# Kernel tuning notes

Measured on AMD Instinct MI355X. Metric: run time of the kernel, lower is better.

Reference implementation:

```python
import jax, jax.numpy as jnp
import numpy as np


def setup_inputs() -> dict:
    key = jax.random.key(0)
    k1, k2 = jax.random.split(key)
    N, C, H, W = 8, 512, 64, 64
    K = 64
    x = jax.random.normal(k1, (N, C, H, W), dtype=jnp.float32)
    y = jax.random.normal(k2, (N, K, H, W), dtype=jnp.float32)
    scale = jnp.zeros((1,), dtype=jnp.float32)
    return {"x": x, "y": y, "scale": scale}


def reference(x, y, scale):
    N, C, H, W = x.shape
    K = y.shape[1]
    HW = H * W
    xq = x.reshape(N, C, HW)            # (N, C, HW) queries (channel-wise)
    yk = y.reshape(N, K, HW)            # (N, K, HW) keys/values
    # energy: (N, C, K)
    energy = jnp.einsum('ncs,nks->nck', xq, yk)
    # inverted max-subtraction: softmax(max_k(E) - E) over last dim
    energy_new = jnp.max(energy, axis=-1, keepdims=True) - energy
    attention = jax.nn.softmax(energy_new, axis=-1)  # (N, C, K)
    out = jnp.einsum('nck,nks->ncs', attention, yk)   # (N, C, HW)
    out = out.reshape(N, C, H, W)
    return x + scale * out
```

## Files before the change

kernel.cpp:

```cpp
#include <hip/hip_runtime.h>

#define N_ 8
#define C_ 512
#define K_ 64
#define HW_ 4096
#define SCHUNK 128
#define NCH 32

typedef __attribute__((ext_vector_type(8))) short short8;
typedef __attribute__((ext_vector_type(4))) float floatx4;

__device__ __forceinline__ short8 cvt8(const float* __restrict__ p){
  float4 u = *(const float4*)p;
  float4 w = *(const float4*)(p + 4);
  union { unsigned u32[4]; short8 s; } r;
  asm("v_cvt_pk_bf16_f32 %0, %1, %2" : "=v"(r.u32[0]) : "v"(u.x), "v"(u.y));
  asm("v_cvt_pk_bf16_f32 %0, %1, %2" : "=v"(r.u32[1]) : "v"(u.z), "v"(u.w));
  asm("v_cvt_pk_bf16_f32 %0, %1, %2" : "=v"(r.u32[2]) : "v"(w.x), "v"(w.y));
  asm("v_cvt_pk_bf16_f32 %0, %1, %2" : "=v"(r.u32[3]) : "v"(w.z), "v"(w.w));
  return r.s;
}

__device__ __forceinline__ void gload16(const void* g, void* l){
  __builtin_amdgcn_global_load_lds(
      (const __attribute__((address_space(1))) void*)g,
      (__attribute__((address_space(3))) void*)l, 16, 0, 0);
}

__global__ __launch_bounds__(256) void k_prep(const float* __restrict__ y,
                                              unsigned short* __restrict__ ybf,
                                              unsigned short* __restrict__ ytr){
  __shared__ unsigned short tile[64][72];
  int n  = blockIdx.x >> 6;
  int s0 = (blockIdx.x & 63) << 6;
  int tid = threadIdx.x;
  int k  = tid >> 2;
  int sc = (tid & 3) << 4;
  const float* yp = y + ((size_t)n * K_ + k) * HW_ + s0 + sc;
  union { unsigned short u16[16]; short8 s8[2]; uint4 q[2]; } u;
  u.s8[0] = cvt8(yp);
  u.s8[1] = cvt8(yp + 8);
  unsigned short* rp = ybf + ((size_t)n * K_ + k) * HW_ + s0 + sc;
  *(uint4*)rp       = u.q[0];
  *(uint4*)(rp + 8) = u.q[1];
#pragma unroll
  for (int j = 0; j < 16; ++j) tile[sc + j][k] = u.u16[j];
  __syncthreads();
  int s  = tid >> 2;
  int kc = (tid & 3) << 4;
  unsigned short* tp = ytr + ((size_t)n * HW_ + s0 + s) * K_ + kc;
  *(uint4*)tp       = *(const uint4*)&tile[s][kc];
  *(uint4*)(tp + 8) = *(const uint4*)&tile[s][kc + 8];
}

__global__ __launch_bounds__(1024) void k_fused(const float* __restrict__ x,
                                                const unsigned short* __restrict__ ybf,
                                                const unsigned short* __restrict__ ytr,
                                                const float* __restrict__ scale,
                                                float* __restrict__ out){
  __shared__ char smem[116736];

  const int bid = ((blockIdx.x & 7) << 5) | (blockIdx.x >> 3);
  const int ct = bid & 31, n = bid >> 5;
  const int tid = threadIdx.x;
  const int w = tid >> 6, l = tid & 63;
  const int lo = l & 15, hi = l >> 4;
  const int h = w >> 2, q = w & 3;
  const int c0 = ct << 4;

  float sc = scale[0];
  asm volatile("" :: "v"(sc));

  const int ar = l >> 3;
  const int ag = (l & 7) ^ ar;
  const char* asrc0 = (const char*)(x + ((size_t)n * C_ + c0 + 0 + ar) * HW_
                                    + h * 32 + ag * 4);
  const char* asrc1 = (const char*)(x + ((size_t)n * C_ + c0 + 8 + ar) * HW_
                                    + h * 32 + ag * 4);
  const int br = l >> 2;
  const int bg = (l & 3) ^ (br & 3);
  const char* bsrc = (const char*)(ybf + ((size_t)n * K_ + (q << 4) + br) * HW_
                                   + h * 32 + bg * 8);

  char* wbase = smem + w * 6144;
  floatx4 acc = {0.f, 0.f, 0.f, 0.f};

#define ESTG(BUF, CH)                                                          \
  {                                                                            \
    gload16(asrc0 + (size_t)(CH) * (SCHUNK * 4), wbase + (BUF) * 3072);        \
    gload16(asrc1 + (size_t)(CH) * (SCHUNK * 4), wbase + (BUF) * 3072 + 1024); \
    gload16(bsrc  + (size_t)(CH) * (SCHUNK * 2), wbase + (BUF) * 3072 + 2048); \
  }

#define ECMP(BUF)                                                              \
  {                                                                            \
    const char* Ab = wbase + (BUF) * 3072;                                     \
    float4 f0 = *(const float4*)(Ab + lo * 128 + (((hi << 1)       ^ (lo & 7)) << 4)); \
    float4 f1 = *(const float4*)(Ab + lo * 128 + ((((hi << 1) | 1) ^ (lo & 7)) << 4)); \
    union { unsigned u32[4]; short8 s; } xf;                                   \
    asm("v_cvt_pk_bf16_f32 %0, %1, %2" : "=v"(xf.u32[0]) : "v"(f0.x), "v"(f0.y)); \
    asm("v_cvt_pk_bf16_f32 %0, %1, %2" : "=v"(xf.u32[1]) : "v"(f0.z), "v"(f0.w)); \
    asm("v_cvt_pk_bf16_f32 %0, %1, %2" : "=v"(xf.u32[2]) : "v"(f1.x), "v"(f1.y)); \
    asm("v_cvt_pk_bf16_f32 %0, %1, %2" : "=v"(xf.u32[3]) : "v"(f1.z), "v"(f1.w)); \
    short8 yf = *(const short8*)(Ab + 2048 + lo * 64 + ((hi ^ (lo & 3)) << 4)); \
       \
    acc = __builtin_amdgcn_mfma_f32_16x16x32_bf16(yf, xf.s, acc, 0, 0, 0);     \
  }

  ESTG(0, 0) ESTG(1, 1)

  for (int cp = 0; cp < 15; ++cp){
    int ch = cp << 1;
    asm volatile("s_waitcnt vmcnt(3)" ::: "memory");
    ECMP(0)
    ESTG(0, ch + 2)
    asm volatile("s_waitcnt vmcnt(3)" ::: "memory");
    ECMP(1)
    ESTG(1, ch + 3)
  }
  asm volatile("s_waitcnt vmcnt(3)" ::: "memory");
  ECMP(0)
  asm volatile("s_waitcnt vmcnt(0)" ::: "memory");
  ECMP(1)
#undef ESTG
#undef ECMP

  float (*Els)[16][64] = (float (*)[16][64])(smem + 98304);
  *(floatx4*)&Els[h][lo][(q << 4) + (hi << 2)] = acc;
  __syncthreads();

  char* attl = smem + 114688;
  if (tid < 256){
    int c = tid >> 4, j = tid & 15;
    float4 t0 = *(const float4*)&Els[0][c][4 * j];
    float4 t1 = *(const float4*)&Els[1][c][4 * j];
    float4 t2 = *(const float4*)&Els[2][c][4 * j];
    float4 t3 = *(const float4*)&Els[3][c][4 * j];
    float e0 = t0.x + t1.x + t2.x + t3.x;
    float e1 = t0.y + t1.y + t2.y + t3.y;
    float e2 = t0.z + t1.z + t2.z + t3.z;
    float e3 = t0.w + t1.w + t2.w + t3.w;
    float m = fminf(fminf(e0, e1), fminf(e2, e3));
#pragma unroll
    for (int off = 8; off; off >>= 1) m = fminf(m, __shfl_xor(m, off, 16));
    float p0 = __expf(m - e0), p1 = __expf(m - e1);
    float p2 = __expf(m - e2), p3 = __expf(m - e3);
    float s = p0 + p1 + p2 + p3;
#pragma unroll
    for (int off = 8; off; off >>= 1) s += __shfl_xor(s, off, 16);
    float inv = 1.f / s;
    unsigned d0, d1;
    asm("v_cvt_pk_bf16_f32 %0, %1, %2" : "=v"(d0) : "v"(p0 * inv), "v"(p1 * inv));
    asm("v_cvt_pk_bf16_f32 %0, %1, %2" : "=v"(d1) : "v"(p2 * inv), "v"(p3 * inv));
    uint2 dd; dd.x = d0; dd.y = d1;
    *(uint2*)(attl + c * 128 + ((8 * j) ^ ((c & 7) << 4))) = dd;
  }
  __syncthreads();

  short8 batt0 = *(const short8*)(attl + lo * 128 + ((     hi * 16) ^ ((lo & 7) << 4)));
  short8 batt1 = *(const short8*)(attl + lo * 128 + ((64 + hi * 16) ^ ((lo & 7) << 4)));
  const unsigned short* ybn = ytr + (size_t)n * HW_ * K_;
  const int sP = w << 8;
  float (*Tw)[68] = (float (*)[68])(smem + w * 4352);
  size_t xb[4];
#pragma unroll
  for (int rg = 0; rg < 4; ++rg)
    xb[rg] = ((size_t)n * C_ + c0 + (rg << 2) + hi) * HW_ + sP + (lo << 2);

  short8 aA[8]; float4 xA[4];
  short8 aB[8]; float4 xB[4];

#define PVLOAD(G, AV, XV)                                                      \
  {                                                                            \
    int sg = sP + (G) * 64;                                                    \
    _Pragma("unroll")                                                          \
    for (int t = 0; t < 4; ++t){                                               \
      const unsigned short* ap = ybn + (size_t)(sg + t * 16 + lo) * K_ + (hi << 3); \
      AV[2 * t]     = *(const short8*)(ap);                                    \
      AV[2 * t + 1] = *(const short8*)(ap + 32);                               \
    }                                                                          \
    _Pragma("unroll")                                                          \
    for (int rg = 0; rg < 4; ++rg)                                             \
      XV[rg] = *(const float4*)(x + xb[rg] + (G) * 64);                        \
  }

#define PVCOMP(G, AV, XV)                                                      \
  {                                                                            \
    _Pragma("unroll")                                                          \
    for (int t = 0; t < 4; ++t){                                               \
      floatx4 a2 = {0.f, 0.f, 0.f, 0.f};                                       \
      a2 = __builtin_amdgcn_mfma_f32_16x16x32_bf16(AV[2 * t],     batt0, a2, 0, 0, 0); \
      a2 = __builtin_amdgcn_mfma_f32_16x16x32_bf16(AV[2 * t + 1], batt1, a2, 0, 0, 0); \
      *(floatx4*)&Tw[lo][t * 16 + (hi << 2)] = a2;    \
    }                                                                          \
    _Pragma("unroll")                                                          \
    for (int rg = 0; rg < 4; ++rg){                                            \
      float4 v  = *(const float4*)&Tw[(rg << 2) + hi][lo << 2];                \
      float4 xv = XV[rg];                                                      \
      float4 o;                                                                \
      o.x = xv.x + sc * v.x; o.y = xv.y + sc * v.y;                            \
      o.z = xv.z + sc * v.z; o.w = xv.w + sc * v.w;                            \
      *(float4*)(out + xb[rg] + (G) * 64) = o;                                 \
    }                                                                          \
  }

  PVLOAD(0, aA, xA)
  PVLOAD(1, aB, xB)
  PVCOMP(0, aA, xA)
  PVLOAD(2, aA, xA)
  PVCOMP(1, aB, xB)
  PVLOAD(3, aB, xB)
  PVCOMP(2, aA, xA)
  PVCOMP(3, aB, xB)
#undef PVLOAD
#undef PVCOMP
}

extern "C" void kernel_launch(void* const* d_in, const int* in_sizes, int n_in,
                              void* d_out, int out_size, void* d_ws, size_t ws_size,
                              hipStream_t stream){
  const float* x     = (const float*)d_in[0];
  const float* y     = (const float*)d_in[1];
  const float* scale = (const float*)d_in[2];
  float* out = (float*)d_out;

  char* ws = (char*)d_ws;
  unsigned short* ybf = (unsigned short*)(ws);
  unsigned short* ytr = (unsigned short*)(ws + (4u<<20));

  k_prep  <<<N_ * (HW_/64), 256,  0, stream>>>(y, ybf, ytr);
  k_fused <<<N_ * 32,       1024, 0, stream>>>(x, ybf, ytr, scale, out);
}
```

Measured before the change: 49.00 us.

## Split fused kernel into split-HW energy and parallel PV kernels

Replaces the single fused kernel (256 blocks of 1024 threads) with two kernels. The energy kernel splits the HW reduction into two halves and writes partial energies to workspace. A separate PV kernel with 2048 blocks of 256 threads sums the partials, computes the softmax, and applies the attention over eight HW slices. This aims to raise occupancy and parallelism across CUs, at the cost of an extra launch, a workspace round-trip, and softmax being recomputed by every slice block.

After: 49.92 us. About the same (+1.9%).

```diff
diff --git a/kernel.cpp b/kernel.cpp
--- a/kernel.cpp
+++ b/kernel.cpp
@@ -4,8 +4,6 @@
 #define C_ 512
 #define K_ 64
 #define HW_ 4096
-#define SCHUNK 128
-#define NCH 32
 
 typedef __attribute__((ext_vector_type(8))) short short8;
 typedef __attribute__((ext_vector_type(4))) float floatx4;
@@ -53,43 +51,38 @@
   *(uint4*)(tp + 8) = *(const uint4*)&tile[s][kc + 8];
 }
 
-__global__ __launch_bounds__(1024) void k_fused(const float* __restrict__ x,
-                                                const unsigned short* __restrict__ ybf,
-                                                const unsigned short* __restrict__ ytr,
-                                                const float* __restrict__ scale,
-                                                float* __restrict__ out){
-  __shared__ char smem[116736];
-
-  const int bid = ((blockIdx.x & 7) << 5) | (blockIdx.x >> 3);
-  const int ct = bid & 31, n = bid >> 5;
+__global__ __launch_bounds__(512) void k_esm(const float* __restrict__ x,
+                                             const unsigned short* __restrict__ ybf,
+                                             float* __restrict__ partial){
+  __shared__ char smem[49152];
+  const int bid = ((blockIdx.x & 7) << 6) | (blockIdx.x >> 3);
+  const int half = bid & 1, ct = (bid >> 1) & 31, n = bid >> 6;
   const int tid = threadIdx.x;
   const int w = tid >> 6, l = tid & 63;
   const int lo = l & 15, hi = l >> 4;
   const int h = w >> 2, q = w & 3;
   const int c0 = ct << 4;
-
-  float sc = scale[0];
-  asm volatile("" :: "v"(sc));
+  const int sb = half << 11;
 
   const int ar = l >> 3;
   const int ag = (l & 7) ^ ar;
   const char* asrc0 = (const char*)(x + ((size_t)n * C_ + c0 + 0 + ar) * HW_
-                                    + h * 32 + ag * 4);
+                                    + sb + h * 32 + ag * 4);
   const char* asrc1 = (const char*)(x + ((size_t)n * C_ + c0 + 8 + ar) * HW_
-                                    + h * 32 + ag * 4);
+                                    + sb + h * 32 + ag * 4);
   const int br = l >> 2;
   const int bg = (l & 3) ^ (br & 3);
   const char* bsrc = (const char*)(ybf + ((size_t)n * K_ + (q << 4) + br) * HW_
-                                   + h * 32 + bg * 8);
+                                   + sb + h * 32 + bg * 8);
 
   char* wbase = smem + w * 6144;
   floatx4 acc = {0.f, 0.f, 0.f, 0.f};
 
 #define ESTG(BUF, CH)                                                          \
   {                                                                            \
-    gload16(asrc0 + (size_t)(CH) * (SCHUNK * 4), wbase + (BUF) * 3072);        \
-    gload16(asrc1 + (size_t)(CH) * (SCHUNK * 4), wbase + (BUF) * 3072 + 1024); \
-    gload16(bsrc  + (size_t)(CH) * (SCHUNK * 2), wbase + (BUF) * 3072 + 2048); \
+    gload16(asrc0 + (size_t)(CH) * 256, wbase + (BUF) * 3072);                 \
+    gload16(asrc1 + (size_t)(CH) * 256, wbase + (BUF) * 3072 + 1024);          \
+    gload16(bsrc  + (size_t)(CH) * 128, wbase + (BUF) * 3072 + 2048);          \
   }
 
 #define ECMP(BUF)                                                              \
@@ -125,43 +118,42 @@
 #undef ESTG
 #undef ECMP
 
-  float (*Els)[16][64] = (float (*)[16][64])(smem + 98304);
+  __syncthreads();
+  float (*Els)[16][64] = (float (*)[16][64])smem;
   *(floatx4*)&Els[h][lo][(q << 4) + (hi << 2)] = acc;
   __syncthreads();
 
-  char* attl = smem + 114688;
   if (tid < 256){
     int c = tid >> 4, j = tid & 15;
     float4 t0 = *(const float4*)&Els[0][c][4 * j];
     float4 t1 = *(const float4*)&Els[1][c][4 * j];
-    float4 t2 = *(const float4*)&Els[2][c][4 * j];
-    float4 t3 = *(const float4*)&Els[3][c][4 * j];
-    float e0 = t0.x + t1.x + t2.x + t3.x;
-    float e1 = t0.y + t1.y + t2.y + t3.y;
-    float e2 = t0.z + t1.z + t2.z + t3.z;
-    float e3 = t0.w + t1.w + t2.w + t3.w;
-    float m = fminf(fminf(e0, e1), fminf(e2, e3));
-#pragma unroll
-    for (int off = 8; off; off >>= 1) m = fminf(m, __shfl_xor(m, off, 16));
-    float p0 = __expf(m - e0), p1 = __expf(m - e1);
-    float p2 = __expf(m - e2), p3 = __expf(m - e3);
-    float s = p0 + p1 + p2 + p3;
-#pragma unroll
-    for (int off = 8; off; off >>= 1) s += __shfl_xor(s, off, 16);
-    float inv = 1.f / s;
-    unsigned d0, d1;
-    asm("v_cvt_pk_bf16_f32 %0, %1, %2" : "=v"(d0) : "v"(p0 * inv), "v"(p1 * inv));
-    asm("v_cvt_pk_bf16_f32 %0, %1, %2" : "=v"(d1) : "v"(p2 * inv), "v"(p3 * inv));
-    uint2 dd; dd.x = d0; dd.y = d1;
-    *(uint2*)(attl + c * 128 + ((8 * j) ^ ((c & 7) << 4))) = dd;
-  }
-  __syncthreads();
-
-  short8 batt0 = *(const short8*)(attl + lo * 128 + ((     hi * 16) ^ ((lo & 7) << 4)));
-  short8 batt1 = *(const short8*)(attl + lo * 128 + ((64 + hi * 16) ^ ((lo & 7) << 4)));
+    float4 e;
+    e.x = t0.x + t1.x; e.y = t0.y + t1.y;
+    e.z = t0.z + t1.z; e.w = t0.w + t1.w;
+    *(float4*)(partial + (((size_t)(half * N_ + n)) * C_ + c0 + c) * K_ + 4 * j) = e;
+  }
+}
+
+__global__ __launch_bounds__(256) void k_pv(const float* __restrict__ x,
+                                            const float* __restrict__ partial,
+                                            const unsigned short* __restrict__ ytr,
+                                            const float* __restrict__ scale,
+                                            float* __restrict__ out){
+  __shared__ float T[4][16][68];
+  __shared__ char attl[2048];
+  int bid = ((blockIdx.x & 7) << 8) | (blockIdx.x >> 3);
+  int sb = bid & 7;
+  int ct = (bid >> 3) & 31;
+  int n  = bid >> 8;
+  int tid = threadIdx.x;
+  int w  = tid >> 6;
+  int l  = tid & 63, lo = l & 15, hi = l >> 4;
+  int c0 = ct << 4;
+  int sP = (sb << 9) + (w << 7);
+  float sc = scale[0];
+
   const unsigned short* ybn = ytr + (size_t)n * HW_ * K_;
-  const int sP = w << 8;
-  float (*Tw)[68] = (float (*)[68])(smem + w * 4352);
+  float (*Tw)[68] = T[w];
   size_t xb[4];
 #pragma unroll
   for (int rg = 0; rg < 4; ++rg)
@@ -205,13 +197,36 @@
   }
 
   PVLOAD(0, aA, xA)
+
+  {
+    int c = tid >> 4, j = tid & 15;
+    const float* pp = partial + ((size_t)n * C_ + c0 + c) * K_ + 4 * j;
+    float4 t0 = *(const float4*)(pp);
+    float4 t1 = *(const float4*)(pp + (size_t)N_ * C_ * K_);
+    float e0 = t0.x + t1.x, e1 = t0.y + t1.y, e2 = t0.z + t1.z, e3 = t0.w + t1.w;
+    float m = fminf(fminf(e0, e1), fminf(e2, e3));
+#pragma unroll
+    for (int off = 8; off; off >>= 1) m = fminf(m, __shfl_xor(m, off, 16));
+    float p0 = __expf(m - e0), p1 = __expf(m - e1);
+    float p2 = __expf(m - e2), p3 = __expf(m - e3);
+    float s = p0 + p1 + p2 + p3;
+#pragma unroll
+    for (int off = 8; off; off >>= 1) s += __shfl_xor(s, off, 16);
+    float inv = 1.f / s;
+    unsigned d0, d1;
+    asm("v_cvt_pk_bf16_f32 %0, %1, %2" : "=v"(d0) : "v"(p0 * inv), "v"(p1 * inv));
+    asm("v_cvt_pk_bf16_f32 %0, %1, %2" : "=v"(d1) : "v"(p2 * inv), "v"(p3 * inv));
+    uint2 dd; dd.x = d0; dd.y = d1;
+    *(uint2*)(attl + c * 128 + ((8 * j) ^ ((c & 7) << 4))) = dd;
+  }
+  __syncthreads();
+
+  short8 batt0 = *(const short8*)(attl + lo * 128 + ((     hi * 16) ^ ((lo & 7) << 4)));
+  short8 batt1 = *(const short8*)(attl + lo * 128 + ((64 + hi * 16) ^ ((lo & 7) << 4)));
+
   PVLOAD(1, aB, xB)
   PVCOMP(0, aA, xA)
-  PVLOAD(2, aA, xA)
   PVCOMP(1, aB, xB)
-  PVLOAD(3, aB, xB)
-  PVCOMP(2, aA, xA)
-  PVCOMP(3, aB, xB)
 #undef PVLOAD
 #undef PVCOMP
 }
@@ -225,9 +240,11 @@
   float* out = (float*)d_out;
 
   char* ws = (char*)d_ws;
-  unsigned short* ybf = (unsigned short*)(ws);
-  unsigned short* ytr = (unsigned short*)(ws + (4u<<20));
-
-  k_prep  <<<N_ * (HW_/64), 256,  0, stream>>>(y, ybf, ytr);
-  k_fused <<<N_ * 32,       1024, 0, stream>>>(x, ybf, ytr, scale, out);
-}
+  float*          partial = (float*)(ws);
+  unsigned short* ybf     = (unsigned short*)(ws + (2u<<20));
+  unsigned short* ytr     = (unsigned short*)(ws + (6u<<20));
+
+  k_prep <<<N_ * (HW_/64), 256, 0, stream>>>(y, ybf, ytr);
+  k_esm  <<<N_ * 32 * 2,   512, 0, stream>>>(x, ybf, partial);
+  k_pv   <<<N_ * 32 * 8,   256, 0, stream>>>(x, partial, ytr, scale, out);
+}
```
